# Performance work log

Measured on AMD Instinct MI355X. Metric: run time of the kernel, lower is better.

## Reference

```python
import jax, jax.numpy as jnp
import numpy as np

NHEAD = 3
NPTS = 5
HID = 96
B_GRAPHS = 16384
COORDS_WEIGHT = 1.0


def _ln(x, g, b):
    mu = jnp.mean(x, -1, keepdims=True)
    v = jnp.mean((x - mu) ** 2, -1, keepdims=True)
    return (x - mu) / jnp.sqrt(v + 1e-5) * g + b


def _build_edge_index():
    # fully-connected per graph, grouped by source node (row-major over sources)
    idx = np.arange(NPTS)
    src = np.repeat(idx, NPTS - 1)
    dst = np.concatenate([np.delete(idx, i) for i in range(NPTS)])
    off = (np.arange(B_GRAPHS) * NPTS)[:, None]
    row = (off + src[None, :]).reshape(-1)
    col = (off + dst[None, :]).reshape(-1)
    return jnp.asarray(np.stack([row, col]), dtype=jnp.int32)


def setup_inputs():
    key = jax.random.key(0)
    ks = jax.random.split(key, 24)
    Nn = B_GRAPHS * NPTS          # 81920 nodes
    E = B_GRAPHS * NPTS * (NPTS - 1)  # 327680 edges

    def w(k, i, o):
        return jax.random.normal(k, (i, o), jnp.float32) * (1.0 / np.sqrt(i))

    inp = {
        'h': jax.random.normal(ks[0], (Nn, HID), jnp.float32),
        'edge_index': _build_edge_index(),
        'coord': jax.random.normal(ks[1], (Nn, 3), jnp.float32),
        'coord_pre': jax.random.normal(ks[2], (Nn, 3), jnp.float32),
        'vel': jax.random.normal(ks[3], (Nn, 3), jnp.float32),
        'edge_attr': jax.random.normal(ks[4], (E, HID), jnp.float32),
        # edge_mlp
        'ew1': w(ks[5], 3 * HID, HID), 'eb1': jnp.zeros((HID,), jnp.float32),
        'ew2': w(ks[6], HID, HID), 'eb2': jnp.zeros((HID,), jnp.float32),
        # edge_mlp_enhance
        'xw1': w(ks[7], 3 * HID, HID), 'xb1': jnp.zeros((HID,), jnp.float32),
        'xw2': w(ks[8], HID, HID), 'xb2': jnp.zeros((HID,), jnp.float32),
        # node_mlp
        'nw1': w(ks[9], 2 * HID, HID), 'nb1': jnp.zeros((HID,), jnp.float32),
        'nw2': w(ks[10], HID, HID), 'nb2': jnp.zeros((HID,), jnp.float32),
        # coord_mlp_inner
        'cw1': w(ks[11], HID, HID), 'cb1': jnp.zeros((HID,), jnp.float32),
        'cw2': w(ks[12], HID, HID), 'cb2': jnp.zeros((HID,), jnp.float32),
        'cw3': w(ks[13], HID, 3), 'cb3': jnp.zeros((3,), jnp.float32),
        # attention projections
        'qw': w(ks[14], HID, HID), 'qb': jnp.zeros((HID,), jnp.float32),
        'kw': w(ks[15], 2 * HID, HID), 'kb': jnp.zeros((HID,), jnp.float32),
        'vw': w(ks[16], HID, HID), 'vb': jnp.zeros((HID,), jnp.float32),
        # layernorms
        'g1': jnp.ones((HID,), jnp.float32), 'be1': jnp.zeros((HID,), jnp.float32),
        'g2': jnp.ones((HID,), jnp.float32), 'be2': jnp.zeros((HID,), jnp.float32),
    }
    return inp


def _forward(h, edge_index, coord, coord_pre, vel, edge_attr,
             ew1, eb1, ew2, eb2, xw1, xb1, xw2, xb2, nw1, nb1, nw2, nb2,
             cw1, cb1, cw2, cb2, cw3, cb3, qw, qb, kw, kb, vw, vb,
             g1, be1, g2, be2):
    sp = jax.nn.softplus
    row, col = edge_index[0], edge_index[1]
    n_nodes = h.shape[0]

    # edge_model (attention flag is False)
    ef = sp(jnp.concatenate([h[row], h[col], edge_attr], 1) @ ew1 + eb1)
    ef = sp(ef @ ew2 + eb2)  # [E, C]

    B, N, C = n_nodes // NPTS, NPTS, ef.shape[-1]
    d = C // NHEAD
    q = h.reshape(B, N, C)
    m = ef.reshape(B, N, N - 1, C)
    h_m = jnp.concatenate(
        [jnp.broadcast_to(q[:, :, None, :], (B, N, N - 1, C)), m], -1
    ).reshape(B, N * (N - 1), 2 * C)

    qh = (q @ qw + qb).reshape(B, N, NHEAD, d).transpose(0, 2, 1, 3)           # [B,H,N,d]
    kh = (h_m @ kw + kb).reshape(B, N * (N - 1), NHEAD, d).transpose(0, 2, 1, 3)
    kh = kh.reshape(B, NHEAD, N, N - 1, d)                                      # [B,H,N,N-1,d]
    vh = (ef.reshape(B, N * (N - 1), C) @ vw + vb).reshape(B, N * (N - 1), NHEAD, d).transpose(0, 2, 1, 3)

    scores = jnp.einsum('bhnd,bhnkd->bhnk', qh, kh) / jnp.sqrt(jnp.float32(d))
    attw = jax.nn.softmax(scores, -1)                                           # [B,H,N,N-1]
    m_update = attw.reshape(B, NHEAD, N * (N - 1), 1) * vh                      # [B,H,E',d]
    att_edge_feat = m_update.transpose(0, 2, 1, 3).reshape(-1, C)               # [E, C]

    # node_model
    agg = jax.ops.segment_sum(att_edge_feat, row, num_segments=n_nodes)
    agg = _ln(agg, g1, be1)
    out = sp(jnp.concatenate([h, agg], 1) @ nw1 + nb1) @ nw2 + nb2
    hn = _ln(h + out, g2, be2)

    # edge enhance
    ef2 = ef + (sp(jnp.concatenate([hn[row], hn[col], edge_attr], 1) @ xw1 + xb1) @ xw2 + xb2)

    # coord2radial on coord_pre (norm_diff=False)
    cd = coord_pre[row] - coord_pre[col]
    cc = jnp.cross(coord_pre[row], coord_pre[col])
    cv = jnp.cross(cd, cc)

    # acc_model_inner
    t = sp(ef2 @ cw1 + cb1)
    t = sp(t @ cw2 + cb2)
    bc = t @ cw3 + cb3                                                          # [E, 3]
    trans = jnp.clip(cd * bc[:, :1] + cc * bc[:, 1:2] + cv * bc[:, 2:3], -100.0, 100.0)
    s = jax.ops.segment_sum(trans, row, num_segments=n_nodes)
    cnt = jax.ops.segment_sum(jnp.ones_like(trans), row, num_segments=n_nodes)
    acc = (s / jnp.maximum(cnt, 1.0)) * COORDS_WEIGHT

    return acc, hn, ef2


def reference(h, edge_index, coord, coord_pre, vel, edge_attr,
              ew1, eb1, ew2, eb2, xw1, xb1, xw2, xb2, nw1, nb1, nw2, nb2,
              cw1, cb1, cw2, cb2, cw3, cb3, qw, qb, kw, kb, vw, vb,
              g1, be1, g2, be2):
    return _forward(h, edge_index, coord, coord_pre, vel, edge_attr,
                    ew1, eb1, ew2, eb2, xw1, xb1, xw2, xb2, nw1, nb1, nw2, nb2,
                    cw1, cb1, cw2, cb2, cw3, cb3, qw, qb, kw, kb, vw, vb,
                    g1, be1, g2, be2)
```

## Files before the change

kernel.cpp:

```cpp
#include <hip/hip_runtime.h>
#include <hip/hip_bf16.h>

#define B_GRAPHS 16384
#define NN (B_GRAPHS * 5)
#define NE (NN * 4)
#define GPB 4
#define EPB 80
#define NPB 20

typedef __attribute__((ext_vector_type(8))) short bf8;
typedef __attribute__((ext_vector_type(4))) short s4;
typedef __attribute__((ext_vector_type(4))) float f4;
typedef __attribute__((ext_vector_type(2))) unsigned u2;
typedef __attribute__((ext_vector_type(4))) unsigned u4;

#define OFF_EW1 0
#define OFF_EW2 27648
#define OFF_KW  36864
#define OFF_VW  55296
#define OFF_QW  64512
#define OFF_NW1 73728
#define OFF_NW2 92160
#define OFF_XW1 101376
#define OFF_XW2 129024
#define OFF_CW1 138240
#define OFF_CW2 147456

__device__ __forceinline__ float sp_f(float x) {
    return fmaxf(x, 0.0f) + __logf(1.0f + __expf(-fabsf(x)));
}
__device__ __forceinline__ short tobf(float x) {
    return __builtin_bit_cast(short, __float2bfloat16(x));
}
__device__ __forceinline__ float frombf(short s) {
    union { float f; unsigned u; } v;
    v.u = ((unsigned)(unsigned short)s) << 16;
    return v.f;
}
__device__ __forceinline__ unsigned pk2(float a, float b) {
    unsigned lo = (unsigned short)tobf(a);
    unsigned hi = (unsigned short)tobf(b);
    return lo | (hi << 16);
}
__device__ __forceinline__ bf8 ldfrag(const short* buf, int row, int k) {
    return *(const bf8*)&buf[(row * 96 + k) ^ ((row & 7) << 3)];
}
__device__ __forceinline__ void stpk(short* buf, int row, int col0, f4 v) {
    u2 o = {pk2(v[0], v[1]), pk2(v[2], v[3])};
    *(u2*)&buf[(row * 96 + col0) ^ ((row & 7) << 3)] = o;
}
__device__ __forceinline__ void stpk8(short* buf, int row, int col0,
                                      const float* v) {
    u4 o = {pk2(v[0], v[1]), pk2(v[2], v[3]), pk2(v[4], v[5]), pk2(v[6], v[7])};
    *(u4*)&buf[(row * 96 + col0) ^ ((row & 7) << 3)] = o;
}

template <int K, int NS, class AF>
__device__ __forceinline__ void gemmCol(const short* __restrict__ wT, int wc0,
                                        int ln, int kg, AF aload, f4* acc) {
    constexpr int NK = K / 32;
    bf8 wf[NK];
    const short* wp = wT + (size_t)(wc0 + ln) * K + kg * 8;
#pragma unroll
    for (int kk = 0; kk < NK; kk++) wf[kk] = *(const bf8*)(wp + kk * 32);
#pragma unroll
    for (int s = 0; s < NS; s++) {
        acc[s][0] = 0.f; acc[s][1] = 0.f; acc[s][2] = 0.f; acc[s][3] = 0.f;
    }
#pragma unroll
    for (int kk = 0; kk < NK; kk++) {
#pragma unroll
        for (int s = 0; s < NS; s++) {
            acc[s] = __builtin_amdgcn_mfma_f32_16x16x32_bf16(wf[kk],
                                                             aload(s, kk * 32),
                                                             acc[s], 0, 0, 0);
        }
    }
}

__global__ __launch_bounds__(256) void k_prep(
    const float* ew1, const float* ew2, const float* kw, const float* vw,
    const float* qw, const float* nw1, const float* nw2, const float* xw1,
    const float* xw2, const float* cw1, const float* cw2, short* wsT) {
    const float* srcs[11] = {ew1, ew2, kw, vw, qw, nw1, nw2, xw1, xw2, cw1, cw2};
    const int Ks[11] = {288, 96, 192, 96, 96, 192, 96, 288, 96, 96, 96};
    const int offs[11] = {OFF_EW1, OFF_EW2, OFF_KW, OFF_VW, OFF_QW, OFF_NW1,
                          OFF_NW2, OFF_XW1, OFF_XW2, OFF_CW1, OFF_CW2};
    int b = blockIdx.x;
    const float* src = srcs[b];
    int K = Ks[b], off = offs[b];
    for (int idx = threadIdx.x; idx < K * 96; idx += 256) {
        int n = idx / K, k = idx - n * K;
        wsT[off + idx] = tobf(src[(size_t)k * 96 + n]);
    }
}

__global__ __launch_bounds__(384, 4) void k_fused(
    const float* __restrict__ h, const float* __restrict__ cp,
    const float* __restrict__ ea, const short* __restrict__ wsT,
    const float* __restrict__ eb1, const float* __restrict__ eb2,
    const float* __restrict__ qb, const float* __restrict__ kb,
    const float* __restrict__ vb, const float* __restrict__ nb1,
    const float* __restrict__ nb2, const float* __restrict__ g1,
    const float* __restrict__ be1, const float* __restrict__ g2,
    const float* __restrict__ be2, const float* __restrict__ xb1,
    const float* __restrict__ xb2, const float* __restrict__ cb1,
    const float* __restrict__ cb2, const float* __restrict__ cw3,
    const float* __restrict__ cb3,
    float* __restrict__ accg, float* __restrict__ hng, float* __restrict__ efg) {
    __shared__ __align__(16) short smem[19680];
    short* hb = smem;
    short* SB = smem + 1920;
    short* E1 = smem + 3840;
    short* E2 = smem + 11520;
    float* sc   = (float*)(smem + 19200);
    float* bcb  = sc;
    float* cw3s = (float*)SB;
    float* trs  = (float*)(SB + 640);

    const int t = threadIdx.x;
    const int blk = blockIdx.x;
    const int n0 = blk * NPB, e0 = blk * EPB;

    for (int i = t; i < 1920; i += 384) {
        int r = i / 24, c = (i - r * 24) * 4;
        f4 v = *(const f4*)&ea[(size_t)(e0 + r) * 96 + c];
        stpk(E2, r, c, v);
    }
    for (int i = t; i < 480; i += 384) {
        int r = i / 24, c = (i - r * 24) * 4;
        f4 v = *(const f4*)&h[(size_t)(n0 + r) * 96 + c];
        stpk(hb, r, c, v);
    }
    __syncthreads();

    const int lane = t & 63, w = t >> 6;
    const int kg = lane >> 4, ln = lane & 15;
    const int wc0 = w * 16, col0 = wc0 + kg * 4;

    int erow[5], esrc[5], edst[5];
#pragma unroll
    for (int s = 0; s < 5; s++) {
        erow[s] = s * 16 + ln;
        int sl = erow[s] >> 2;
        esrc[s] = sl;
        int si = sl % 5, jj = erow[s] & 3;
        edst[s] = (sl / 5) * 5 + jj + (jj >= si);
    }

    f4 acc[5];
    gemmCol<288, 5>(wsT + OFF_EW1, wc0, ln, kg,
        [&](int s, int k0) -> bf8 {
            int k = k0 + kg * 8;
            if (k0 < 96)  return ldfrag(hb, esrc[s], k);
            if (k0 < 192) return ldfrag(hb, edst[s], k - 96);
            return ldfrag(E2, erow[s], k - 192);
        }, acc);
    {
        f4 b = *(const f4*)&eb1[col0];
#pragma unroll
        for (int s = 0; s < 5; s++) {
            f4 v;
#pragma unroll
            for (int j = 0; j < 4; j++) v[j] = sp_f(acc[s][j] + b[j]);
            stpk(E1, erow[s], col0, v);
        }
    }
    __syncthreads();
    gemmCol<96, 5>(wsT + OFF_EW2, wc0, ln, kg,
        [&](int s, int k0) { return ldfrag(E1, erow[s], k0 + kg * 8); }, acc);
    {
        f4 qa[2];
        gemmCol<96, 2>(wsT + OFF_QW, wc0, ln, kg,
            [&](int s, int k0) { return ldfrag(hb, s * 16 + ln, k0 + kg * 8); }, qa);
        f4 b = *(const f4*)&eb2[col0];
#pragma unroll
        for (int s = 0; s < 5; s++) {
            f4 v;
#pragma unroll
            for (int j = 0; j < 4; j++) v[j] = sp_f(acc[s][j] + b[j]);
            stpk(E2, erow[s], col0, v);
        }
        f4 bq = *(const f4*)&qb[col0];
#pragma unroll
        for (int s = 0; s < 2; s++) {
            int row = s * 16 + ln;
            if (row < NPB) {
                f4 v;
#pragma unroll
                for (int j = 0; j < 4; j++) v[j] = qa[s][j] + bq[j];
                stpk(SB, row, col0, v);
            }
        }
    }
    __syncthreads();
    gemmCol<192, 5>(wsT + OFF_KW, wc0, ln, kg,
        [&](int s, int k0) {
            int k = k0 + kg * 8;
            if (k0 < 96) return ldfrag(hb, esrc[s], k);
            return ldfrag(E2, erow[s], k - 96);
        }, acc);
    {
        f4 b = *(const f4*)&kb[col0];
#pragma unroll
        for (int s = 0; s < 5; s++) {
            f4 v;
#pragma unroll
            for (int j = 0; j < 4; j++) v[j] = acc[s][j] + b[j];
            stpk(E1, erow[s], col0, v);
        }
    }
    __syncthreads();
    if (t < 240) {
        int e = t / 3, hd = t - e * 3, nd = e >> 2;
        float s = 0.f;
#pragma unroll
        for (int c8 = 0; c8 < 4; c8++) {
            int c = hd * 32 + c8 * 8;
            bf8 qv = ldfrag(SB, nd, c);
            bf8 kv = ldfrag(E1, e, c);
#pragma unroll
            for (int j = 0; j < 8; j++) s = fmaf(frombf(qv[j]), frombf(kv[j]), s);
        }
        sc[e * 3 + hd] = s * 0.17677669529663687f;
    }
    __syncthreads();
    if (t < 60) {
        int nd = t / 3, hd = t - nd * 3;
        float v0 = sc[(nd * 4 + 0) * 3 + hd], v1 = sc[(nd * 4 + 1) * 3 + hd];
        float v2 = sc[(nd * 4 + 2) * 3 + hd], v3 = sc[(nd * 4 + 3) * 3 + hd];
        float m = fmaxf(fmaxf(v0, v1), fmaxf(v2, v3));
        float p0 = __expf(v0 - m), p1 = __expf(v1 - m);
        float p2 = __expf(v2 - m), p3 = __expf(v3 - m);
        float inv = 1.f / (p0 + p1 + p2 + p3);
        sc[(nd * 4 + 0) * 3 + hd] = p0 * inv;
        sc[(nd * 4 + 1) * 3 + hd] = p1 * inv;
        sc[(nd * 4 + 2) * 3 + hd] = p2 * inv;
        sc[(nd * 4 + 3) * 3 + hd] = p3 * inv;
    }
    gemmCol<96, 5>(wsT + OFF_VW, wc0, ln, kg,
        [&](int s, int k0) { return ldfrag(E2, erow[s], k0 + kg * 8); }, acc);
    {
        f4 b = *(const f4*)&vb[col0];
#pragma unroll
        for (int s = 0; s < 5; s++) {
            f4 v;
#pragma unroll
            for (int j = 0; j < 4; j++) v[j] = acc[s][j] + b[j];
            stpk(E1, erow[s], col0, v);
        }
    }
    __syncthreads();
    if (t < 320) {
        int nd = t >> 4, cg = t & 15;
        bool act = cg < 12;
        int hd = cg >> 2;
        float agg[8];
#pragma unroll
        for (int j = 0; j < 8; j++) agg[j] = 0.f;
        if (act) {
#pragma unroll
            for (int k = 0; k < 4; k++) {
                int e = nd * 4 + k;
                float wgt = sc[e * 3 + hd];
                bf8 v8 = ldfrag(E1, e, cg * 8);
#pragma unroll
                for (int j = 0; j < 8; j++) agg[j] = fmaf(wgt, frombf(v8[j]), agg[j]);
            }
        }
        float s1 = 0.f, s2 = 0.f;
#pragma unroll
        for (int j = 0; j < 8; j++) { s1 += agg[j]; s2 += agg[j] * agg[j]; }
        if (!act) { s1 = 0.f; s2 = 0.f; }
        for (int m = 1; m < 16; m <<= 1) {
            s1 += __shfl_xor(s1, m);
            s2 += __shfl_xor(s2, m);
        }
        float mu = s1 * (1.f / 96.f);
        float var = s2 * (1.f / 96.f) - mu * mu;
        float rs = rsqrtf(var + 1e-5f);
        if (act) {
            int c = cg * 8;
            f4 ga = *(const f4*)&g1[c], gb = *(const f4*)&g1[c + 4];
            f4 ba = *(const f4*)&be1[c], bb = *(const f4*)&be1[c + 4];
            float o[8];
#pragma unroll
            for (int j = 0; j < 4; j++) {
                o[j] = (agg[j] - mu) * rs * ga[j] + ba[j];
                o[j + 4] = (agg[j + 4] - mu) * rs * gb[j] + bb[j];
            }
            stpk8(SB, nd, c, o);
        }
    }
    __syncthreads();
    {
        f4 eav[5];
        int rr[5], cc[5];
#pragma unroll
        for (int u = 0; u < 5; u++) {
            int i = t + u * 384;
            rr[u] = i / 24; cc[u] = (i - rr[u] * 24) * 4;
            eav[u] = *(const f4*)&ea[(size_t)(e0 + rr[u]) * 96 + cc[u]];
        }
        f4 na[2];
        gemmCol<192, 2>(wsT + OFF_NW1, wc0, ln, kg,
            [&](int s, int k0) {
                int row = s * 16 + ln, k = k0 + kg * 8;
                if (k0 < 96) return ldfrag(hb, row, k);
                return ldfrag(SB, row, k - 96);
            }, na);
        f4 b = *(const f4*)&nb1[col0];
        f4 t1v[2];
#pragma unroll
        for (int s = 0; s < 2; s++)
#pragma unroll
            for (int j = 0; j < 4; j++) t1v[s][j] = sp_f(na[s][j] + b[j]);
        __syncthreads();
#pragma unroll
        for (int s = 0; s < 2; s++) {
            int row = s * 16 + ln;
            if (row < NPB) stpk(SB, row, col0, t1v[s]);
        }
#pragma unroll
        for (int u = 0; u < 5; u++) stpk(E1, rr[u], cc[u], eav[u]);
    }
    __syncthreads();
    {
        f4 na[2];
        gemmCol<96, 2>(wsT + OFF_NW2, wc0, ln, kg,
            [&](int s, int k0) { return ldfrag(SB, s * 16 + ln, k0 + kg * 8); }, na);
        f4 b = *(const f4*)&nb2[col0];
#pragma unroll
        for (int s = 0; s < 2; s++) {
            int row = s * 16 + ln;
            if (row < NPB) {
                f4 hv = *(const f4*)&h[(size_t)(n0 + row) * 96 + col0];
                f4 v;
#pragma unroll
                for (int j = 0; j < 4; j++) v[j] = na[s][j] + b[j] + hv[j];
                stpk(hb, row, col0, v);
            }
        }
    }
    __syncthreads();
    if (t < 320) {
        int nd = t >> 4, cg = t & 15;
        bool act = cg < 12;
        float xv[8];
#pragma unroll
        for (int j = 0; j < 8; j++) xv[j] = 0.f;
        if (act) {
            bf8 x = ldfrag(hb, nd, cg * 8);
#pragma unroll
            for (int j = 0; j < 8; j++) xv[j] = frombf(x[j]);
        }
        float s1 = 0.f, s2 = 0.f;
#pragma unroll
        for (int j = 0; j < 8; j++) { s1 += xv[j]; s2 += xv[j] * xv[j]; }
        for (int m = 1; m < 16; m <<= 1) {
            s1 += __shfl_xor(s1, m);
            s2 += __shfl_xor(s2, m);
        }
        float mu = s1 * (1.f / 96.f);
        float var = s2 * (1.f / 96.f) - mu * mu;
        float rs = rsqrtf(var + 1e-5f);
        if (act) {
            int c = cg * 8;
            f4 ga = *(const f4*)&g2[c], gb = *(const f4*)&g2[c + 4];
            f4 ba = *(const f4*)&be2[c], bb = *(const f4*)&be2[c + 4];
            float o[8];
#pragma unroll
            for (int j = 0; j < 4; j++) {
                o[j] = (xv[j] - mu) * rs * ga[j] + ba[j];
                o[j + 4] = (xv[j + 4] - mu) * rs * gb[j] + bb[j];
            }
            f4 o0 = {o[0], o[1], o[2], o[3]}, o1 = {o[4], o[5], o[6], o[7]};
            *(f4*)&hng[(size_t)(n0 + nd) * 96 + c] = o0;
            *(f4*)&hng[(size_t)(n0 + nd) * 96 + c + 4] = o1;
            stpk8(hb, nd, c, o);
        }
    }
    __syncthreads();
    gemmCol<288, 5>(wsT + OFF_XW1, wc0, ln, kg,
        [&](int s, int k0) -> bf8 {
            int k = k0 + kg * 8;
            if (k0 < 96)  return ldfrag(hb, esrc[s], k);
            if (k0 < 192) return ldfrag(hb, edst[s], k - 96);
            return ldfrag(E1, erow[s], k - 192);
        }, acc);
    __syncthreads();
    {
        f4 b = *(const f4*)&xb1[col0];
#pragma unroll
        for (int s = 0; s < 5; s++) {
            f4 v;
#pragma unroll
            for (int j = 0; j < 4; j++) v[j] = sp_f(acc[s][j] + b[j]);
            stpk(E1, erow[s], col0, v);
        }
    }
    __syncthreads();
    gemmCol<96, 5>(wsT + OFF_XW2, wc0, ln, kg,
        [&](int s, int k0) { return ldfrag(E1, erow[s], k0 + kg * 8); }, acc);
    {
        f4 b = *(const f4*)&xb2[col0];
#pragma unroll
        for (int s = 0; s < 5; s++) {
            int row = erow[s];
            s4 ev = *(const s4*)&E2[(row * 96 + col0) ^ ((row & 7) << 3)];
            f4 v;
#pragma unroll
            for (int j = 0; j < 4; j++) v[j] = acc[s][j] + b[j] + frombf(ev[j]);
            *(f4*)&efg[(size_t)(e0 + row) * 96 + col0] = v;
            stpk(E2, row, col0, v);
        }
    }
    __syncthreads();
    gemmCol<96, 5>(wsT + OFF_CW1, wc0, ln, kg,
        [&](int s, int k0) { return ldfrag(E2, erow[s], k0 + kg * 8); }, acc);
    {
        f4 b = *(const f4*)&cb1[col0];
#pragma unroll
        for (int s = 0; s < 5; s++) {
            f4 v;
#pragma unroll
            for (int j = 0; j < 4; j++) v[j] = sp_f(acc[s][j] + b[j]);
            stpk(E1, erow[s], col0, v);
        }
    }
    __syncthreads();
    if (t < 288) cw3s[t] = cw3[t];
    gemmCol<96, 5>(wsT + OFF_CW2, wc0, ln, kg,
        [&](int s, int k0) { return ldfrag(E1, erow[s], k0 + kg * 8); }, acc);
    {
        f4 b = *(const f4*)&cb2[col0];
#pragma unroll
        for (int s = 0; s < 5; s++) {
            f4 v;
#pragma unroll
            for (int j = 0; j < 4; j++) v[j] = sp_f(acc[s][j] + b[j]);
            stpk(E2, erow[s], col0, v);
        }
    }
    __syncthreads();
    if (t < 240) {
        int e = t / 3, j = t - e * 3;
        float s = cb3[j];
#pragma unroll
        for (int c8 = 0; c8 < 12; c8++) {
            bf8 av = ldfrag(E2, e, c8 * 8);
#pragma unroll
            for (int jj = 0; jj < 8; jj++)
                s = fmaf(frombf(av[jj]), cw3s[(c8 * 8 + jj) * 3 + j], s);
        }
        bcb[e * 3 + j] = s;
    }
    __syncthreads();
    if (t < 80) {
        int sl = t >> 2, jj = t & 3, si = sl % 5;
        int dl = (sl / 5) * 5 + jj + (jj >= si);
        int rn = n0 + sl, cn = n0 + dl;
        float r0c = cp[(size_t)rn * 3 + 0], r1c = cp[(size_t)rn * 3 + 1],
              r2c = cp[(size_t)rn * 3 + 2];
        float q0 = cp[(size_t)cn * 3 + 0], q1 = cp[(size_t)cn * 3 + 1],
              q2 = cp[(size_t)cn * 3 + 2];
        float d0 = r0c - q0, d1 = r1c - q1, d2 = r2c - q2;
        float x0 = r1c * q2 - r2c * q1;
        float x1 = r2c * q0 - r0c * q2;
        float x2 = r0c * q1 - r1c * q0;
        float v0 = d1 * x2 - d2 * x1;
        float v1 = d2 * x0 - d0 * x2;
        float v2 = d0 * x1 - d1 * x0;
        float b0 = bcb[t * 3 + 0], b1 = bcb[t * 3 + 1], b2 = bcb[t * 3 + 2];
        trs[t * 4 + 0] = fminf(fmaxf(d0 * b0 + x0 * b1 + v0 * b2, -100.f), 100.f);
        trs[t * 4 + 1] = fminf(fmaxf(d1 * b0 + x1 * b1 + v1 * b2, -100.f), 100.f);
        trs[t * 4 + 2] = fminf(fmaxf(d2 * b0 + x2 * b1 + v2 * b2, -100.f), 100.f);
    }
    __syncthreads();
    if (t < 60) {
        int nd = t / 3, j = t - nd * 3;
        float s = (trs[(nd * 4 + 0) * 4 + j] + trs[(nd * 4 + 1) * 4 + j] +
                   trs[(nd * 4 + 2) * 4 + j] + trs[(nd * 4 + 3) * 4 + j]) * 0.25f;
        accg[(size_t)(n0 + nd) * 3 + j] = s;
    }
}

extern "C" void kernel_launch(void* const* d_in, const int* in_sizes, int n_in,
                              void* d_out, int out_size, void* d_ws, size_t ws_size,
                              hipStream_t stream) {
    const float* h   = (const float*)d_in[0];
    const float* cp  = (const float*)d_in[3];
    const float* ea  = (const float*)d_in[5];
    const float* ew1 = (const float*)d_in[6];
    const float* eb1 = (const float*)d_in[7];
    const float* ew2 = (const float*)d_in[8];
    const float* eb2 = (const float*)d_in[9];
    const float* xw1 = (const float*)d_in[10];
    const float* xb1 = (const float*)d_in[11];
    const float* xw2 = (const float*)d_in[12];
    const float* xb2 = (const float*)d_in[13];
    const float* nw1 = (const float*)d_in[14];
    const float* nb1 = (const float*)d_in[15];
    const float* nw2 = (const float*)d_in[16];
    const float* nb2 = (const float*)d_in[17];
    const float* cw1 = (const float*)d_in[18];
    const float* cb1 = (const float*)d_in[19];
    const float* cw2 = (const float*)d_in[20];
    const float* cb2 = (const float*)d_in[21];
    const float* cw3 = (const float*)d_in[22];
    const float* cb3 = (const float*)d_in[23];
    const float* qw  = (const float*)d_in[24];
    const float* qb  = (const float*)d_in[25];
    const float* kw  = (const float*)d_in[26];
    const float* kb  = (const float*)d_in[27];
    const float* vw  = (const float*)d_in[28];
    const float* vb  = (const float*)d_in[29];
    const float* g1  = (const float*)d_in[30];
    const float* be1 = (const float*)d_in[31];
    const float* g2  = (const float*)d_in[32];
    const float* be2 = (const float*)d_in[33];

    float* out  = (float*)d_out;
    float* accg = out;
    float* hng  = out + (size_t)NN * 3;
    float* efg  = out + (size_t)NN * 3 + (size_t)NN * 96;
    short* wsT = (short*)d_ws;

    k_prep<<<11, 256, 0, stream>>>(ew1, ew2, kw, vw, qw, nw1, nw2, xw1, xw2,
                                   cw1, cw2, wsT);
    k_fused<<<B_GRAPHS / GPB, 384, 0, stream>>>(
        h, cp, ea, wsT, eb1, eb2, qb, kb, vb, nb1, nb2, g1, be1, g2, be2,
        xb1, xb2, cb1, cb2, cw3, cb3, accg, hng, efg);
}
```

Measured before the change: 393.6 us.

## Halve graphs per block, fuse softmax via shuffles, merge coord stages

Each block now handles 2 graphs (40 edges, 10 nodes) instead of 4. This cuts LDS use and per-thread accumulator count (3 MFMA row tiles instead of 5) so more blocks can be resident. The attention softmax now runs inside the score pass using wave shuffles, and the coord-MLP final projection is merged with the translation computation, which removes several barriers. bf16 packing uses the v_cvt_pk_bf16_f32 instruction. The trade-off is padded MFMA tiles (48 rows computed for 40 real edges) and twice as many blocks, each reloading the weights.

New measurement: 462.6 us. 1.18x slower.

```diff
diff --git a/kernel.cpp b/kernel.cpp
--- a/kernel.cpp
+++ b/kernel.cpp
@@ -4,9 +4,10 @@
 #define B_GRAPHS 16384
 #define NN (B_GRAPHS * 5)
 #define NE (NN * 4)
-#define GPB 4
-#define EPB 80
-#define NPB 20
+#define GPB 2
+#define EPB 40
+#define NPB 10
+#define EST 3
 
 typedef __attribute__((ext_vector_type(8))) short bf8;
 typedef __attribute__((ext_vector_type(4))) short s4;
@@ -38,9 +39,9 @@
     return v.f;
 }
 __device__ __forceinline__ unsigned pk2(float a, float b) {
-    unsigned lo = (unsigned short)tobf(a);
-    unsigned hi = (unsigned short)tobf(b);
-    return lo | (hi << 16);
+    unsigned r;
+    asm("v_cvt_pk_bf16_f32 %0, %1, %2" : "=v"(r) : "v"(a), "v"(b));
+    return r;
 }
 __device__ __forceinline__ bf8 ldfrag(const short* buf, int row, int k) {
     return *(const bf8*)&buf[(row * 96 + k) ^ ((row & 7) << 3)];
@@ -53,6 +54,11 @@
                                       const float* v) {
     u4 o = {pk2(v[0], v[1]), pk2(v[2], v[3]), pk2(v[4], v[5]), pk2(v[6], v[7])};
     *(u4*)&buf[(row * 96 + col0) ^ ((row & 7) << 3)] = o;
+}
+__device__ __forceinline__ int esrc_of(int er) { return er >> 2; }
+__device__ __forceinline__ int edst_of(int er) {
+    int sl = er >> 2, si = sl % 5, jj = er & 3;
+    return (sl / 5) * 5 + jj + (jj >= si);
 }
 
 template <int K, int NS, class AF>
@@ -108,27 +114,26 @@
     const float* __restrict__ cb2, const float* __restrict__ cw3,
     const float* __restrict__ cb3,
     float* __restrict__ accg, float* __restrict__ hng, float* __restrict__ efg) {
-    __shared__ __align__(16) short smem[19680];
+    __shared__ __align__(16) short smem[13488];
     short* hb = smem;
-    short* SB = smem + 1920;
-    short* E1 = smem + 3840;
-    short* E2 = smem + 11520;
-    float* sc   = (float*)(smem + 19200);
-    float* bcb  = sc;
+    short* SB = smem + 1536;
+    short* E1 = smem + 4032;
+    short* E2 = smem + 8640;
+    float* sc   = (float*)(smem + 13248);
     float* cw3s = (float*)SB;
-    float* trs  = (float*)(SB + 640);
+    float* trs  = (float*)(SB + 10 * 96);
 
     const int t = threadIdx.x;
     const int blk = blockIdx.x;
     const int n0 = blk * NPB, e0 = blk * EPB;
 
-    for (int i = t; i < 1920; i += 384) {
+    for (int i = t; i < EPB * 24; i += 384) {
         int r = i / 24, c = (i - r * 24) * 4;
         f4 v = *(const f4*)&ea[(size_t)(e0 + r) * 96 + c];
         stpk(E2, r, c, v);
     }
-    for (int i = t; i < 480; i += 384) {
-        int r = i / 24, c = (i - r * 24) * 4;
+    if (t < NPB * 24) {
+        int r = t / 24, c = (t - r * 24) * 4;
         f4 v = *(const f4*)&h[(size_t)(n0 + r) * 96 + c];
         stpk(hb, r, c, v);
     }
@@ -138,18 +143,17 @@
     const int kg = lane >> 4, ln = lane & 15;
     const int wc0 = w * 16, col0 = wc0 + kg * 4;
 
-    int erow[5], esrc[5], edst[5];
-#pragma unroll
-    for (int s = 0; s < 5; s++) {
+    int erow[EST], esrc[EST], edst[EST];
+#pragma unroll
+    for (int s = 0; s < EST; s++) {
         erow[s] = s * 16 + ln;
-        int sl = erow[s] >> 2;
-        esrc[s] = sl;
-        int si = sl % 5, jj = erow[s] & 3;
-        edst[s] = (sl / 5) * 5 + jj + (jj >= si);
-    }
-
-    f4 acc[5];
-    gemmCol<288, 5>(wsT + OFF_EW1, wc0, ln, kg,
+        int er = erow[s] < EPB ? erow[s] : 0;
+        esrc[s] = esrc_of(er);
+        edst[s] = edst_of(er);
+    }
+
+    f4 acc[EST];
+    gemmCol<288, EST>(wsT + OFF_EW1, wc0, ln, kg,
         [&](int s, int k0) -> bf8 {
             int k = k0 + kg * 8;
             if (k0 < 96)  return ldfrag(hb, esrc[s], k);
@@ -159,7 +163,7 @@
     {
         f4 b = *(const f4*)&eb1[col0];
 #pragma unroll
-        for (int s = 0; s < 5; s++) {
+        for (int s = 0; s < EST; s++) {
             f4 v;
 #pragma unroll
             for (int j = 0; j < 4; j++) v[j] = sp_f(acc[s][j] + b[j]);
@@ -167,34 +171,30 @@
         }
     }
     __syncthreads();
-    gemmCol<96, 5>(wsT + OFF_EW2, wc0, ln, kg,
+    gemmCol<96, EST>(wsT + OFF_EW2, wc0, ln, kg,
         [&](int s, int k0) { return ldfrag(E1, erow[s], k0 + kg * 8); }, acc);
     {
-        f4 qa[2];
-        gemmCol<96, 2>(wsT + OFF_QW, wc0, ln, kg,
-            [&](int s, int k0) { return ldfrag(hb, s * 16 + ln, k0 + kg * 8); }, qa);
+        f4 qa[1];
+        gemmCol<96, 1>(wsT + OFF_QW, wc0, ln, kg,
+            [&](int s, int k0) { return ldfrag(hb, ln, k0 + kg * 8); }, qa);
         f4 b = *(const f4*)&eb2[col0];
 #pragma unroll
-        for (int s = 0; s < 5; s++) {
+        for (int s = 0; s < EST; s++) {
             f4 v;
 #pragma unroll
             for (int j = 0; j < 4; j++) v[j] = sp_f(acc[s][j] + b[j]);
             stpk(E2, erow[s], col0, v);
         }
         f4 bq = *(const f4*)&qb[col0];
-#pragma unroll
-        for (int s = 0; s < 2; s++) {
-            int row = s * 16 + ln;
-            if (row < NPB) {
-                f4 v;
-#pragma unroll
-                for (int j = 0; j < 4; j++) v[j] = qa[s][j] + bq[j];
-                stpk(SB, row, col0, v);
-            }
-        }
-    }
-    __syncthreads();
-    gemmCol<192, 5>(wsT + OFF_KW, wc0, ln, kg,
+        if (ln < NPB) {
+            f4 v;
+#pragma unroll
+            for (int j = 0; j < 4; j++) v[j] = qa[0][j] + bq[j];
+            stpk(SB, ln, col0, v);
+        }
+    }
+    __syncthreads();
+    gemmCol<192, EST>(wsT + OFF_KW, wc0, ln, kg,
         [&](int s, int k0) {
             int k = k0 + kg * 8;
             if (k0 < 96) return ldfrag(hb, esrc[s], k);
@@ -203,7 +203,7 @@
     {
         f4 b = *(const f4*)&kb[col0];
 #pragma unroll
-        for (int s = 0; s < 5; s++) {
+        for (int s = 0; s < EST; s++) {
             f4 v;
 #pragma unroll
             for (int j = 0; j < 4; j++) v[j] = acc[s][j] + b[j];
@@ -211,39 +211,40 @@
         }
     }
     __syncthreads();
-    if (t < 240) {
-        int e = t / 3, hd = t - e * 3, nd = e >> 2;
+    {
+        int nd = w * 4 + (lane / 12);
+        bool act = (lane < 48) && (nd < NPB);
+        int rem = lane % 12, hd = rem >> 2, k4 = rem & 3;
+        int e = (nd < NPB ? nd : 0) * 4 + k4;
         float s = 0.f;
-#pragma unroll
-        for (int c8 = 0; c8 < 4; c8++) {
-            int c = hd * 32 + c8 * 8;
-            bf8 qv = ldfrag(SB, nd, c);
-            bf8 kv = ldfrag(E1, e, c);
-#pragma unroll
-            for (int j = 0; j < 8; j++) s = fmaf(frombf(qv[j]), frombf(kv[j]), s);
-        }
-        sc[e * 3 + hd] = s * 0.17677669529663687f;
-    }
-    __syncthreads();
-    if (t < 60) {
-        int nd = t / 3, hd = t - nd * 3;
-        float v0 = sc[(nd * 4 + 0) * 3 + hd], v1 = sc[(nd * 4 + 1) * 3 + hd];
-        float v2 = sc[(nd * 4 + 2) * 3 + hd], v3 = sc[(nd * 4 + 3) * 3 + hd];
-        float m = fmaxf(fmaxf(v0, v1), fmaxf(v2, v3));
-        float p0 = __expf(v0 - m), p1 = __expf(v1 - m);
-        float p2 = __expf(v2 - m), p3 = __expf(v3 - m);
-        float inv = 1.f / (p0 + p1 + p2 + p3);
-        sc[(nd * 4 + 0) * 3 + hd] = p0 * inv;
-        sc[(nd * 4 + 1) * 3 + hd] = p1 * inv;
-        sc[(nd * 4 + 2) * 3 + hd] = p2 * inv;
-        sc[(nd * 4 + 3) * 3 + hd] = p3 * inv;
-    }
-    gemmCol<96, 5>(wsT + OFF_VW, wc0, ln, kg,
+        if (act) {
+#pragma unroll
+            for (int c8 = 0; c8 < 4; c8++) {
+                int c = hd * 32 + c8 * 8;
+                bf8 qv = ldfrag(SB, nd, c);
+                bf8 kv = ldfrag(E1, e, c);
+#pragma unroll
+                for (int j = 0; j < 8; j++)
+                    s = fmaf(frombf(qv[j]), frombf(kv[j]), s);
+            }
+            s *= 0.17677669529663687f;
+        }
+        float m = s;
+        m = fmaxf(m, __shfl_xor(m, 1));
+        m = fmaxf(m, __shfl_xor(m, 2));
+        float p = act ? __expf(s - m) : 0.f;
+        float sum = p;
+        sum += __shfl_xor(sum, 1);
+        sum += __shfl_xor(sum, 2);
+        if (act) sc[e * 3 + hd] = p / sum;
+    }
+    __syncthreads();
+    gemmCol<96, EST>(wsT + OFF_VW, wc0, ln, kg,
         [&](int s, int k0) { return ldfrag(E2, erow[s], k0 + kg * 8); }, acc);
     {
         f4 b = *(const f4*)&vb[col0];
 #pragma unroll
-        for (int s = 0; s < 5; s++) {
+        for (int s = 0; s < EST; s++) {
             f4 v;
 #pragma unroll
             for (int j = 0; j < 4; j++) v[j] = acc[s][j] + b[j];
@@ -251,7 +252,7 @@
         }
     }
     __syncthreads();
-    if (t < 320) {
+    if (t < 160) {
         int nd = t >> 4, cg = t & 15;
         bool act = cg < 12;
         int hd = cg >> 2;
@@ -294,63 +295,57 @@
     }
     __syncthreads();
     {
-        f4 eav[5];
-        int rr[5], cc[5];
-#pragma unroll
-        for (int u = 0; u < 5; u++) {
+        f4 eav[3];
+        int rr[3], cc[3];
+        bool ev[3];
+#pragma unroll
+        for (int u = 0; u < 3; u++) {
             int i = t + u * 384;
+            ev[u] = i < EPB * 24;
             rr[u] = i / 24; cc[u] = (i - rr[u] * 24) * 4;
-            eav[u] = *(const f4*)&ea[(size_t)(e0 + rr[u]) * 96 + cc[u]];
-        }
-        f4 na[2];
-        gemmCol<192, 2>(wsT + OFF_NW1, wc0, ln, kg,
+            if (ev[u]) eav[u] = *(const f4*)&ea[(size_t)(e0 + rr[u]) * 96 + cc[u]];
+        }
+        f4 na[1];
+        gemmCol<192, 1>(wsT + OFF_NW1, wc0, ln, kg,
             [&](int s, int k0) {
-                int row = s * 16 + ln, k = k0 + kg * 8;
-                if (k0 < 96) return ldfrag(hb, row, k);
-                return ldfrag(SB, row, k - 96);
+                int k = k0 + kg * 8;
+                if (k0 < 96) return ldfrag(hb, ln, k);
+                return ldfrag(SB, ln, k - 96);
             }, na);
         f4 b = *(const f4*)&nb1[col0];
-        f4 t1v[2];
-#pragma unroll
-        for (int s = 0; s < 2; s++)
-#pragma unroll
-            for (int j = 0; j < 4; j++) t1v[s][j] = sp_f(na[s][j] + b[j]);
-        __syncthreads();
-#pragma unroll
-        for (int s = 0; s < 2; s++) {
-            int row = s * 16 + ln;
-            if (row < NPB) stpk(SB, row, col0, t1v[s]);
-        }
-#pragma unroll
-        for (int u = 0; u < 5; u++) stpk(E1, rr[u], cc[u], eav[u]);
-    }
-    __syncthreads();
-    {
-        f4 na[2];
-        gemmCol<96, 2>(wsT + OFF_NW2, wc0, ln, kg,
-            [&](int s, int k0) { return ldfrag(SB, s * 16 + ln, k0 + kg * 8); }, na);
+        if (ln < NPB) {
+            f4 v;
+#pragma unroll
+            for (int j = 0; j < 4; j++) v[j] = sp_f(na[0][j] + b[j]);
+            stpk(SB, 16 + ln, col0, v);
+        }
+#pragma unroll
+        for (int u = 0; u < 3; u++)
+            if (ev[u]) stpk(E1, rr[u], cc[u], eav[u]);
+    }
+    __syncthreads();
+    {
+        f4 na[1];
+        gemmCol<96, 1>(wsT + OFF_NW2, wc0, ln, kg,
+            [&](int s, int k0) { return ldfrag(SB, 16 + ln, k0 + kg * 8); }, na);
         f4 b = *(const f4*)&nb2[col0];
-#pragma unroll
-        for (int s = 0; s < 2; s++) {
-            int row = s * 16 + ln;
-            if (row < NPB) {
-                f4 hv = *(const f4*)&h[(size_t)(n0 + row) * 96 + col0];
-                f4 v;
-#pragma unroll
-                for (int j = 0; j < 4; j++) v[j] = na[s][j] + b[j] + hv[j];
-                stpk(hb, row, col0, v);
-            }
-        }
-    }
-    __syncthreads();
-    if (t < 320) {
+        if (ln < NPB) {
+            f4 hv = *(const f4*)&h[(size_t)(n0 + ln) * 96 + col0];
+            f4 v;
+#pragma unroll
+            for (int j = 0; j < 4; j++) v[j] = na[0][j] + b[j] + hv[j];
+            stpk(SB, ln, col0, v);
+        }
+    }
+    __syncthreads();
+    if (t < 160) {
         int nd = t >> 4, cg = t & 15;
         bool act = cg < 12;
         float xv[8];
 #pragma unroll
         for (int j = 0; j < 8; j++) xv[j] = 0.f;
         if (act) {
-            bf8 x = ldfrag(hb, nd, cg * 8);
+            bf8 x = ldfrag(SB, nd, cg * 8);
 #pragma unroll
             for (int j = 0; j < 8; j++) xv[j] = frombf(x[j]);
         }
@@ -381,7 +376,7 @@
         }
     }
     __syncthreads();
-    gemmCol<288, 5>(wsT + OFF_XW1, wc0, ln, kg,
+    gemmCol<288, EST>(wsT + OFF_XW1, wc0, ln, kg,
         [&](int s, int k0) -> bf8 {
             int k = k0 + kg * 8;
             if (k0 < 96)  return ldfrag(hb, esrc[s], k);
@@ -392,7 +387,7 @@
     {
         f4 b = *(const f4*)&xb1[col0];
 #pragma unroll
-        for (int s = 0; s < 5; s++) {
+        for (int s = 0; s < EST; s++) {
             f4 v;
 #pragma unroll
             for (int j = 0; j < 4; j++) v[j] = sp_f(acc[s][j] + b[j]);
@@ -400,28 +395,29 @@
         }
     }
     __syncthreads();
-    gemmCol<96, 5>(wsT + OFF_XW2, wc0, ln, kg,
+    gemmCol<96, EST>(wsT + OFF_XW2, wc0, ln, kg,
         [&](int s, int k0) { return ldfrag(E1, erow[s], k0 + kg * 8); }, acc);
     {
         f4 b = *(const f4*)&xb2[col0];
 #pragma unroll
-        for (int s = 0; s < 5; s++) {
+        for (int s = 0; s < EST; s++) {
             int row = erow[s];
             s4 ev = *(const s4*)&E2[(row * 96 + col0) ^ ((row & 7) << 3)];
             f4 v;
 #pragma unroll
             for (int j = 0; j < 4; j++) v[j] = acc[s][j] + b[j] + frombf(ev[j]);
-            *(f4*)&efg[(size_t)(e0 + row) * 96 + col0] = v;
+            if (row < EPB)
+                *(f4*)&efg[(size_t)(e0 + row) * 96 + col0] = v;
             stpk(E2, row, col0, v);
         }
     }
     __syncthreads();
-    gemmCol<96, 5>(wsT + OFF_CW1, wc0, ln, kg,
+    gemmCol<96, EST>(wsT + OFF_CW1, wc0, ln, kg,
         [&](int s, int k0) { return ldfrag(E2, erow[s], k0 + kg * 8); }, acc);
     {
         f4 b = *(const f4*)&cb1[col0];
 #pragma unroll
-        for (int s = 0; s < 5; s++) {
+        for (int s = 0; s < EST; s++) {
             f4 v;
 #pragma unroll
             for (int j = 0; j < 4; j++) v[j] = sp_f(acc[s][j] + b[j]);
@@ -430,12 +426,12 @@
     }
     __syncthreads();
     if (t < 288) cw3s[t] = cw3[t];
-    gemmCol<96, 5>(wsT + OFF_CW2, wc0, ln, kg,
+    gemmCol<96, EST>(wsT + OFF_CW2, wc0, ln, kg,
         [&](int s, int k0) { return ldfrag(E1, erow[s], k0 + kg * 8); }, acc);
     {
         f4 b = *(const f4*)&cb2[col0];
 #pragma unroll
-        for (int s = 0; s < 5; s++) {
+        for (int s = 0; s < EST; s++) {
             f4 v;
 #pragma unroll
             for (int j = 0; j < 4; j++) v[j] = sp_f(acc[s][j] + b[j]);
@@ -443,22 +439,23 @@
         }
     }
     __syncthreads();
-    if (t < 240) {
-        int e = t / 3, j = t - e * 3;
-        float s = cb3[j];
+    if (t < EPB) {
+        int e = t;
+        float b0 = cb3[0], b1 = cb3[1], b2 = cb3[2];
 #pragma unroll
         for (int c8 = 0; c8 < 12; c8++) {
             bf8 av = ldfrag(E2, e, c8 * 8);
 #pragma unroll
-            for (int jj = 0; jj < 8; jj++)
-                s = fmaf(frombf(av[jj]), cw3s[(c8 * 8 + jj) * 3 + j], s);
-        }
-        bcb[e * 3 + j] = s;
-    }
-    __syncthreads();
-    if (t < 80) {
-        int sl = t >> 2, jj = t & 3, si = sl % 5;
-        int dl = (sl / 5) * 5 + jj + (jj >= si);
+            for (int jj = 0; jj < 8; jj++) {
+                float a = frombf(av[jj]);
+                const float* cw = &cw3s[(c8 * 8 + jj) * 3];
+                b0 = fmaf(a, cw[0], b0);
+                b1 = fmaf(a, cw[1], b1);
+                b2 = fmaf(a, cw[2], b2);
+            }
+        }
+        int sl = e >> 2, jj2 = e & 3, si = sl % 5;
+        int dl = (sl / 5) * 5 + jj2 + (jj2 >= si);
         int rn = n0 + sl, cn = n0 + dl;
         float r0c = cp[(size_t)rn * 3 + 0], r1c = cp[(size_t)rn * 3 + 1],
               r2c = cp[(size_t)rn * 3 + 2];
@@ -471,13 +468,12 @@
         float v0 = d1 * x2 - d2 * x1;
         float v1 = d2 * x0 - d0 * x2;
         float v2 = d0 * x1 - d1 * x0;
-        float b0 = bcb[t * 3 + 0], b1 = bcb[t * 3 + 1], b2 = bcb[t * 3 + 2];
-        trs[t * 4 + 0] = fminf(fmaxf(d0 * b0 + x0 * b1 + v0 * b2, -100.f), 100.f);
-        trs[t * 4 + 1] = fminf(fmaxf(d1 * b0 + x1 * b1 + v1 * b2, -100.f), 100.f);
-        trs[t * 4 + 2] = fminf(fmaxf(d2 * b0 + x2 * b1 + v2 * b2, -100.f), 100.f);
-    }
-    __syncthreads();
-    if (t < 60) {
+        trs[e * 4 + 0] = fminf(fmaxf(d0 * b0 + x0 * b1 + v0 * b2, -100.f), 100.f);
+        trs[e * 4 + 1] = fminf(fmaxf(d1 * b0 + x1 * b1 + v1 * b2, -100.f), 100.f);
+        trs[e * 4 + 2] = fminf(fmaxf(d2 * b0 + x2 * b1 + v2 * b2, -100.f), 100.f);
+    }
+    __syncthreads();
+    if (t < NPB * 3) {
         int nd = t / 3, j = t - nd * 3;
         float s = (trs[(nd * 4 + 0) * 4 + j] + trs[(nd * 4 + 1) * 4 + j] +
                    trs[(nd * 4 + 2) * 4 + j] + trs[(nd * 4 + 3) * 4 + j]) * 0.25f;
```
